# Optimization experiments

Hardware: AMD Instinct MI355X
Metric: run time of the kernel (lower is better)

The kernel has to match this reference:

```python
import jax, jax.numpy as jnp
import numpy as np

B, IN_DIM, HID, K, D = 16384, 1024, 2048, 8192, 128
COMMIT = 0.25


def setup_inputs() -> dict:
    key = jax.random.key(0)
    ks = jax.random.split(key, 10)
    s1 = 1.0 / np.sqrt(IN_DIM)
    s2 = 1.0 / np.sqrt(HID)
    s3 = 1.0 / np.sqrt(D)
    return {
        "x": jax.random.uniform(ks[0], (B, IN_DIM), dtype=jnp.float32),
        "W1": jax.random.normal(ks[1], (IN_DIM, HID), dtype=jnp.float32) * s1,
        "b1": jnp.zeros((HID,), jnp.float32),
        "W2": jax.random.normal(ks[2], (HID, D), dtype=jnp.float32) * s2,
        "b2": jnp.zeros((D,), jnp.float32),
        # torch init: uniform(-1/K, 1/K)
        "codebook": jax.random.uniform(ks[3], (K, D), dtype=jnp.float32, minval=-1.0 / K, maxval=1.0 / K),
        "W3": jax.random.normal(ks[4], (D, HID), dtype=jnp.float32) * s3,
        "b3": jnp.zeros((HID,), jnp.float32),
        "W4": jax.random.normal(ks[5], (HID, IN_DIM), dtype=jnp.float32) * s2,
        "b4": jnp.zeros((IN_DIM,), jnp.float32),
    }


def reference(x, W1, b1, W2, b2, codebook, W3, b3, W4, b4):
    # Encoder MLP: [B, IN] -> [B, D]
    h = jax.nn.relu(x @ W1 + b1)
    z = h @ W2 + b2                                   # [B, D]

    # Squared-distance to codebook: ||z||^2 - 2 z C^T + ||C||^2  -> [B, K]
    dists = (jnp.sum(z * z, axis=1, keepdims=True)
             - 2.0 * (z @ codebook.T)
             + jnp.sum(codebook * codebook, axis=1))
    indices = jnp.argmin(dists, axis=1)               # [B]
    z_q = codebook[indices]                            # [B, D]

    # Straight-through estimator
    z_q_st = z + jax.lax.stop_gradient(z_q - z)

    # Decoder MLP: [B, D] -> [B, IN]
    h2 = jax.nn.relu(z_q_st @ W3 + b3)
    recon = jax.nn.sigmoid(h2 @ W4 + b4)

    sg_zq = jax.lax.stop_gradient(z_q)
    mse = jnp.mean(jnp.square(sg_zq - z))
    loss = mse + COMMIT * mse
    return (recon, loss, indices)
```

## Files before the change

### kernel.cpp

```cpp
#include <hip/hip_runtime.h>
#include <hip/hip_bf16.h>


#define B_    16384
#define INDIM 1024
#define HID   2048
#define KCB   8192
#define DDIM  128

#define CAND_CAP 2000000u
#define LBUF_CAP 1024u

typedef __bf16    bf16x8   __attribute__((ext_vector_type(8)));
typedef float     floatx4  __attribute__((ext_vector_type(4)));
typedef double    doublex4 __attribute__((ext_vector_type(4)));
typedef _Float16  half8    __attribute__((ext_vector_type(8)));
typedef __fp16    fp16x2   __attribute__((ext_vector_type(2)));

#define XS 4096.0f
#define WS 8192.0f
#define SCALE_INV 2.9802322387695312e-08

__device__ __forceinline__ unsigned long long pack_key(float d, int code)
{
    unsigned int u = __float_as_uint(d);
    u = (u & 0x80000000u) ? ~u : (u | 0x80000000u);
    return ((unsigned long long)u << 32) | (unsigned int)code;
}

__device__ __forceinline__ unsigned packf(float d)
{
    unsigned u = __float_as_uint(d);
    return (u & 0x80000000u) ? ~u : (u | 0x80000000u);
}
__device__ __forceinline__ float unpackf(unsigned p)
{
    unsigned u = (p & 0x80000000u) ? (p ^ 0x80000000u) : ~p;
    return __uint_as_float(u);
}

__device__ __forceinline__ void gll16(const float* g, float* l)
{
    __builtin_amdgcn_global_load_lds(
        (const __attribute__((address_space(1))) void*)g,
        (__attribute__((address_space(3))) void*)l, 16, 0, 0);
}

template <int ACT, int PMASK>
__launch_bounds__(256)
__global__ void gemm_split_f16(const float* __restrict__ A, const _Float16* __restrict__ Bs_g,
                               const float* __restrict__ bias, float* __restrict__ Cout,
                               int M, int N, int K)
{
    __shared__ float    As[128 * 32];
    __shared__ _Float16 Bsh[64 * 64];

    const int t    = threadIdx.x;
    const int m0   = blockIdx.y * 128, n0 = blockIdx.x * 64;
    const int wave = t >> 6, lane = t & 63;
    const int wr   = (wave >> 1) * 64, wc = (wave & 1) * 32;
    const int quad = lane >> 4, l16 = lane & 15;
    const int lr   = lane >> 3;
    const int lcA  = ((lane & 7) ^ lr) * 4;
    const int slB  = lane & 7;
    const int lrB  = lane >> 3;

    floatx4  accf[4][2];
    doublex4 accd[4][2];
#pragma unroll
    for (int i = 0; i < 4; ++i)
#pragma unroll
        for (int j = 0; j < 2; ++j) {
            accf[i][j] = (floatx4){0.f, 0.f, 0.f, 0.f};
            accd[i][j] = (doublex4){0.0, 0.0, 0.0, 0.0};
        }

    const int NKT = K >> 5;
    for (int kt = 0; kt < NKT; ++kt) {
        const int k0 = kt << 5;
        __syncthreads();
#pragma unroll
        for (int s = 0; s < 4; ++s) {
            int r = wave * 32 + s * 8;
            gll16(A + (size_t)(m0 + r + lr) * K + k0 + lcA, &As[r * 32]);
        }
#pragma unroll
        for (int s = 0; s < 2; ++s) {
            int rb = wave * 16 + s * 8 + lrB;
            int ccs = slB ^ (lrB & 7);
            gll16((const float*)(Bs_g + (size_t)(n0 + rb) * (2 * K) + kt * 64 + ccs * 8),
                  (float*)&Bsh[(wave * 16 + s * 8) * 64]);
        }
        __syncthreads();

        half8 a1[4], a2[4];
#pragma unroll
        for (int i = 0; i < 4; ++i) {
            const int row = wr + i * 16 + l16;
            const int s0  = (2 * quad) ^ (row & 7);
            const int s1  = (2 * quad + 1) ^ (row & 7);
            floatx4 f0 = *(const floatx4*)&As[row * 32 + s0 * 4];
            floatx4 f1 = *(const floatx4*)&As[row * 32 + s1 * 4];
            union { half8 v; fp16x2 h[4]; } u1, u2;
            float sv[8];
#pragma unroll
            for (int q = 0; q < 4; ++q) sv[q] = f0[q] * XS;
#pragma unroll
            for (int q = 0; q < 4; ++q) sv[4 + q] = f1[q] * XS;
#pragma unroll
            for (int q = 0; q < 4; ++q) {
                fp16x2 hi = __builtin_amdgcn_cvt_pkrtz(sv[2 * q], sv[2 * q + 1]);
                u1.h[q] = hi;
                float r0 = sv[2 * q] - (float)hi[0];
                float r1 = sv[2 * q + 1] - (float)hi[1];
                u2.h[q] = __builtin_amdgcn_cvt_pkrtz(r0, r1);
            }
            a1[i] = u1.v; a2[i] = u2.v;
        }
        half8 b1[2], b2[2];
#pragma unroll
        for (int j = 0; j < 2; ++j) {
            const int row = wc + j * 16 + l16;
            b1[j] = *(const half8*)&Bsh[row * 64 + ((0 + quad) ^ (row & 7)) * 8];
            b2[j] = *(const half8*)&Bsh[row * 64 + ((4 + quad) ^ (row & 7)) * 8];
        }
#pragma unroll
        for (int i = 0; i < 4; ++i)
#pragma unroll
            for (int j = 0; j < 2; ++j)
                accf[i][j] = __builtin_amdgcn_mfma_f32_16x16x32_f16(a1[i], b1[j], accf[i][j], 0, 0, 0);
#pragma unroll
        for (int i = 0; i < 4; ++i)
#pragma unroll
            for (int j = 0; j < 2; ++j)
                accf[i][j] = __builtin_amdgcn_mfma_f32_16x16x32_f16(a1[i], b2[j], accf[i][j], 0, 0, 0);
#pragma unroll
        for (int i = 0; i < 4; ++i)
#pragma unroll
            for (int j = 0; j < 2; ++j)
                accf[i][j] = __builtin_amdgcn_mfma_f32_16x16x32_f16(a2[i], b1[j], accf[i][j], 0, 0, 0);

        if ((kt & PMASK) == PMASK) {
#pragma unroll
            for (int i = 0; i < 4; ++i)
#pragma unroll
                for (int j = 0; j < 2; ++j) {
#pragma unroll
                    for (int r = 0; r < 4; ++r)
                        accd[i][j][r] += (double)accf[i][j][r] * SCALE_INV;
                    accf[i][j] = (floatx4){0.f, 0.f, 0.f, 0.f};
                }
        }
    }
    if (NKT & PMASK) {
#pragma unroll
        for (int i = 0; i < 4; ++i)
#pragma unroll
            for (int j = 0; j < 2; ++j)
#pragma unroll
                for (int r = 0; r < 4; ++r)
                    accd[i][j][r] += (double)accf[i][j][r] * SCALE_INV;
    }

#pragma unroll
    for (int i = 0; i < 4; ++i)
#pragma unroll
        for (int j = 0; j < 2; ++j)
#pragma unroll
            for (int r = 0; r < 4; ++r) {
                int row = m0 + wr + i * 16 + quad * 4 + r;
                int col = n0 + wc + j * 16 + l16;
                float f = (float)(accd[i][j][r] + (double)bias[col]);
                if (ACT == 1) f = fmaxf(f, 0.f);
                Cout[(size_t)row * N + col] = f;
            }
}

template <int IM, int ACT, int PMASK, int SPLITOUT>
__launch_bounds__(256)
__global__ void gemm_split_pre(const _Float16* __restrict__ As_g, const _Float16* __restrict__ Bs_g,
                               const float* __restrict__ bias, void* __restrict__ Cp,
                               int M, int N, int K)
{
    __shared__ _Float16 Ash[IM * 32 * 64];
    __shared__ _Float16 Bsh[64 * 64];

    const int t    = threadIdx.x;
    const int nwg  = gridDim.x * gridDim.y;
    int lin = blockIdx.y * gridDim.x + blockIdx.x;
    lin = (lin & 7) * (nwg >> 3) + (lin >> 3);
    const int bx = lin % gridDim.x, by = lin / gridDim.x;
    const int m0   = by * (IM * 32), n0 = bx * 64;
    const int wave = t >> 6, lane = t & 63;
    const int wr   = (wave >> 1) * (IM * 16), wc = (wave & 1) * 32;
    const int quad = lane >> 4, l16 = lane & 15;
    const int slB  = lane & 7;
    const int lrB  = lane >> 3;
    const int ccs  = slB ^ (lrB & 7);

    floatx4  accf[IM][2];
    doublex4 accd[IM][2];
#pragma unroll
    for (int i = 0; i < IM; ++i)
#pragma unroll
        for (int j = 0; j < 2; ++j) {
            accf[i][j] = (floatx4){0.f, 0.f, 0.f, 0.f};
            accd[i][j] = (doublex4){0.0, 0.0, 0.0, 0.0};
        }

    const int NKT = K >> 5;
    for (int kt = 0; kt < NKT; ++kt) {
        __syncthreads();
#pragma unroll
        for (int s = 0; s < IM; ++s) {
            int ra = wave * (IM * 8) + s * 8 + lrB;
            gll16((const float*)(As_g + (size_t)(m0 + ra) * (2 * K) + kt * 64 + ccs * 8),
                  (float*)&Ash[(wave * (IM * 8) + s * 8) * 64]);
        }
#pragma unroll
        for (int s = 0; s < 2; ++s) {
            int rb = wave * 16 + s * 8 + lrB;
            gll16((const float*)(Bs_g + (size_t)(n0 + rb) * (2 * K) + kt * 64 + ccs * 8),
                  (float*)&Bsh[(wave * 16 + s * 8) * 64]);
        }
        __syncthreads();

        half8 a1[IM], a2[IM], b1[2], b2[2];
#pragma unroll
        for (int i = 0; i < IM; ++i) {
            const int row = wr + i * 16 + l16;
            a1[i] = *(const half8*)&Ash[row * 64 + ((0 + quad) ^ (row & 7)) * 8];
            a2[i] = *(const half8*)&Ash[row * 64 + ((4 + quad) ^ (row & 7)) * 8];
        }
#pragma unroll
        for (int j = 0; j < 2; ++j) {
            const int row = wc + j * 16 + l16;
            b1[j] = *(const half8*)&Bsh[row * 64 + ((0 + quad) ^ (row & 7)) * 8];
            b2[j] = *(const half8*)&Bsh[row * 64 + ((4 + quad) ^ (row & 7)) * 8];
        }
#pragma unroll
        for (int i = 0; i < IM; ++i)
#pragma unroll
            for (int j = 0; j < 2; ++j)
                accf[i][j] = __builtin_amdgcn_mfma_f32_16x16x32_f16(a1[i], b1[j], accf[i][j], 0, 0, 0);
#pragma unroll
        for (int i = 0; i < IM; ++i)
#pragma unroll
            for (int j = 0; j < 2; ++j)
                accf[i][j] = __builtin_amdgcn_mfma_f32_16x16x32_f16(a1[i], b2[j], accf[i][j], 0, 0, 0);
#pragma unroll
        for (int i = 0; i < IM; ++i)
#pragma unroll
            for (int j = 0; j < 2; ++j)
                accf[i][j] = __builtin_amdgcn_mfma_f32_16x16x32_f16(a2[i], b1[j], accf[i][j], 0, 0, 0);

        if ((kt & PMASK) == PMASK) {
#pragma unroll
            for (int i = 0; i < IM; ++i)
#pragma unroll
                for (int j = 0; j < 2; ++j) {
#pragma unroll
                    for (int r = 0; r < 4; ++r)
                        accd[i][j][r] += (double)accf[i][j][r] * SCALE_INV;
                    accf[i][j] = (floatx4){0.f, 0.f, 0.f, 0.f};
                }
        }
    }
    if (NKT & PMASK) {
#pragma unroll
        for (int i = 0; i < IM; ++i)
#pragma unroll
            for (int j = 0; j < 2; ++j)
#pragma unroll
                for (int r = 0; r < 4; ++r)
                    accd[i][j][r] += (double)accf[i][j][r] * SCALE_INV;
    }

#pragma unroll
    for (int i = 0; i < IM; ++i)
#pragma unroll
        for (int j = 0; j < 2; ++j)
#pragma unroll
            for (int r = 0; r < 4; ++r) {
                int row = m0 + wr + i * 16 + quad * 4 + r;
                int col = n0 + wc + j * 16 + l16;
                float f = (float)(accd[i][j][r] + (double)bias[col]);
                if (ACT == 1) f = fmaxf(f, 0.f);
                if (SPLITOUT == 1) {
                    float sv = f * XS;
                    _Float16 p0 = (_Float16)sv;
                    _Float16 p1 = (_Float16)(sv - (float)p0);
                    _Float16* hs = (_Float16*)Cp;
                    size_t base = (size_t)row * (2 * (size_t)N)
                                + (size_t)(col >> 5) * 64 + (col & 31);
                    hs[base]      = p0;
                    hs[base + 32] = p1;
                } else {
                    ((float*)Cp)[(size_t)row * N + col] = f;
                }
            }
}

template <int ACT>
__launch_bounds__(256)
__global__ void gemm_bf16_gll(const __bf16* __restrict__ A, const __bf16* __restrict__ BT,
                              const float* __restrict__ bias, void* __restrict__ Cp,
                              int M, int N, int K)
{
    __shared__ __bf16 Asm[128 * 32];
    __shared__ __bf16 Bsm[128 * 32];

    const int t    = threadIdx.x;
    const int nwg  = gridDim.x * gridDim.y;
    int lin = blockIdx.y * gridDim.x + blockIdx.x;
    lin = (lin & 7) * (nwg >> 3) + (lin >> 3);
    const int bx = lin % gridDim.x, by = lin / gridDim.x;
    const int m0   = by * 128, n0 = bx * 128;
    const int wave = t >> 6, lane = t & 63;
    const int wr   = (wave >> 1) * 64, wc = (wave & 1) * 64;
    const int quad = lane >> 4, l16 = lane & 15;
    const int srow = lane >> 2;
    const int schk = lane & 3;

    floatx4 acc[4][4];
#pragma unroll
    for (int i = 0; i < 4; ++i)
#pragma unroll
        for (int j = 0; j < 4; ++j) acc[i][j] = (floatx4){0.f, 0.f, 0.f, 0.f};

    for (int k0 = 0; k0 < K; k0 += 32) {
        __syncthreads();
#pragma unroll
        for (int s = 0; s < 2; ++s) {
            const int rbase = wave * 32 + s * 16;
            const int ra = rbase + srow;
            const int cs = (schk - (ra >> 1)) & 3;
            gll16((const float*)(A + (size_t)(m0 + ra) * K + k0 + cs * 8),
                  (float*)&Asm[rbase * 32]);
        }
#pragma unroll
        for (int s = 0; s < 2; ++s) {
            const int rbase = wave * 32 + s * 16;
            const int rb = rbase + srow;
            const int cs = (schk - (rb >> 1)) & 3;
            gll16((const float*)(BT + (size_t)(n0 + rb) * K + k0 + cs * 8),
                  (float*)&Bsm[rbase * 32]);
        }
        __syncthreads();

        bf16x8 af[4], bfr[4];
#pragma unroll
        for (int i = 0; i < 4; ++i) {
            const int rl = wr + i * 16 + l16;
            const int sl = (quad + (rl >> 1)) & 3;
            af[i] = *(const bf16x8*)&Asm[rl * 32 + sl * 8];
        }
#pragma unroll
        for (int j = 0; j < 4; ++j) {
            const int rl = wc + j * 16 + l16;
            const int sl = (quad + (rl >> 1)) & 3;
            bfr[j] = *(const bf16x8*)&Bsm[rl * 32 + sl * 8];
        }
#pragma unroll
        for (int i = 0; i < 4; ++i)
#pragma unroll
            for (int j = 0; j < 4; ++j)
                acc[i][j] = __builtin_amdgcn_mfma_f32_16x16x32_bf16(af[i], bfr[j], acc[i][j], 0, 0, 0);
    }

#pragma unroll
    for (int i = 0; i < 4; ++i)
#pragma unroll
        for (int j = 0; j < 4; ++j) {
            int col = n0 + wc + j * 16 + l16;
            float b = bias[col];
#pragma unroll
            for (int r = 0; r < 4; ++r) {
                int row = m0 + wr + i * 16 + quad * 4 + r;
                float v = acc[i][j][r] + b;
                if (ACT == 1) {
                    v = fmaxf(v, 0.f);
                    ((__bf16*)Cp)[(size_t)row * N + col] = (__bf16)v;
                } else {
                    v = 1.f / (1.f + __expf(-v));
                    ((float*)Cp)[(size_t)row * N + col] = v;
                }
            }
        }
}

__global__ void split_x(const float* __restrict__ in, _Float16* __restrict__ outS, int n8)
{
    int i = blockIdx.x * 256 + threadIdx.x;
    if (i >= n8) return;
    const int K = INDIM;
    int m  = i / (K / 8);
    int k8 = i % (K / 8);
    int k  = k8 * 8;
    const float* src = in + (size_t)m * K + k;
    floatx4 f0 = *(const floatx4*)(src);
    floatx4 f1 = *(const floatx4*)(src + 4);
    union { half8 v; fp16x2 h[4]; } u1, u2;
    float sv[8];
#pragma unroll
    for (int q = 0; q < 4; ++q) sv[q] = f0[q] * XS;
#pragma unroll
    for (int q = 0; q < 4; ++q) sv[4 + q] = f1[q] * XS;
#pragma unroll
    for (int q = 0; q < 4; ++q) {
        fp16x2 hi = __builtin_amdgcn_cvt_pkrtz(sv[2 * q], sv[2 * q + 1]);
        u1.h[q] = hi;
        float r0 = sv[2 * q] - (float)hi[0];
        float r1 = sv[2 * q + 1] - (float)hi[1];
        u2.h[q] = __builtin_amdgcn_cvt_pkrtz(r0, r1);
    }
    size_t base = (size_t)m * (2 * K) + (size_t)(k >> 5) * 64 + (k & 31);
    *(half8*)(outS + base)      = u1.v;
    *(half8*)(outS + base + 32) = u2.v;
}

__global__ void transpose_split_f16(const float* __restrict__ in, _Float16* __restrict__ outS,
                                    int K, int N)
{
    __shared__ float tile[32][33];
    int k0 = blockIdx.x * 32, n0 = blockIdx.y * 32;
    int tr = threadIdx.x >> 5, tc = threadIdx.x & 31;
#pragma unroll
    for (int s = 0; s < 4; ++s)
        tile[tr + 8 * s][tc] = in[(size_t)(k0 + tr + 8 * s) * N + n0 + tc];
    __syncthreads();
#pragma unroll
    for (int s = 0; s < 4; ++s) {
        int n = n0 + tr + 8 * s;
        int k = k0 + tc;
        float w = tile[tc][tr + 8 * s] * WS;
        _Float16 p0 = (_Float16)w;
        float r = w - (float)p0;
        _Float16 p1 = (_Float16)r;
        size_t base = (size_t)n * (2 * K) + (size_t)(k >> 5) * 64 + (k & 31);
        outS[base]      = p0;
        outS[base + 32] = p1;
    }
}

__global__ void rownorm_kernel(const float* __restrict__ M, float* __restrict__ nrm)
{
    int k = blockIdx.x * 4 + (threadIdx.x >> 6);
    int lane = threadIdx.x & 63;
    float2 c = *(const float2*)(M + (size_t)k * DDIM + lane * 2);
    float q0 = c.x * c.x;
    float q1 = c.y * c.y;
    double s = (double)q0 + (double)q1;
#pragma unroll
    for (int off = 32; off > 0; off >>= 1) s += __shfl_down(s, off);
    if (lane == 0) nrm[k] = (float)s;
}

__global__ void cnmax_kernel(const float* __restrict__ cn, float* __restrict__ out)
{
    __shared__ float red[4];
    int t = threadIdx.x;
    float m = 0.f;
    for (int i = t; i < KCB; i += 256) m = fmaxf(m, cn[i]);
#pragma unroll
    for (int off = 32; off > 0; off >>= 1) m = fmaxf(m, __shfl_down(m, off));
    if ((t & 63) == 0) red[t >> 6] = m;
    __syncthreads();
    if (t == 0) out[0] = fmaxf(fmaxf(red[0], red[1]), fmaxf(red[2], red[3]));
}

__global__ void cvt_half(const float* __restrict__ in, _Float16* __restrict__ out,
                         float scale, int n8)
{
    int i = blockIdx.x * 256 + threadIdx.x;
    if (i >= n8) return;
    const float4 a = *(const float4*)(in + (size_t)i * 8);
    const float4 b = *(const float4*)(in + (size_t)i * 8 + 4);
    half8 h;
    h[0] = (_Float16)(a.x * scale); h[1] = (_Float16)(a.y * scale);
    h[2] = (_Float16)(a.z * scale); h[3] = (_Float16)(a.w * scale);
    h[4] = (_Float16)(b.x * scale); h[5] = (_Float16)(b.y * scale);
    h[6] = (_Float16)(b.z * scale); h[7] = (_Float16)(b.w * scale);
    *(half8*)(out + (size_t)i * 8) = h;
}

__launch_bounds__(256)
__global__ void score_sweep3(const _Float16* __restrict__ zh, const _Float16* __restrict__ ch,
                             const float* __restrict__ nz32, const float* __restrict__ cn32,
                             const float* __restrict__ cnmaxp,
                             unsigned* __restrict__ listCnt, unsigned* __restrict__ list)
{
    __shared__ __align__(16) _Float16 Zs[32 * 128];
    __shared__ __align__(16) _Float16 Cs[128 * 128];
    __shared__ unsigned rowmin[32];
    __shared__ unsigned lbuf[LBUF_CAP];
    __shared__ unsigned lcnt, lbase;

    const int t    = threadIdx.x;
    int bid = blockIdx.x;
    bid = (bid & 7) * ((int)gridDim.x >> 3) + (bid >> 3);
    const int m0   = bid * 32;
    const int wave = t >> 6, lane = t & 63;
    const int quad = lane >> 4, l16 = lane & 15;
    const int srow = lane >> 4, sc = lane & 15;

    if (t == 0) lcnt = 0u;
    if (t < 32) rowmin[t] = 0xFFFFFFFFu;

#pragma unroll
    for (int s = 0; s < 2; ++s) {
        const int rbase = s * 16 + wave * 4;
        const int ra = rbase + srow;
        const int cs = sc ^ ((ra & 7) << 1);
        gll16((const float*)(zh + (size_t)(m0 + ra) * 128 + cs * 8),
              (float*)&Zs[rbase * 128]);
    }
    __syncthreads();

    half8 af[2][4];
#pragma unroll
    for (int i = 0; i < 2; ++i) {
        const int rl = i * 16 + l16;
#pragma unroll
        for (int ks = 0; ks < 4; ++ks) {
            const int cc = (ks * 4 + quad) ^ ((rl & 7) << 1);
            af[i][ks] = *(const half8*)&Zs[rl * 128 + cc * 8];
        }
    }

    const float cnm = *cnmaxp;
    float nzv[8], W[8];
    unsigned cachemin[8];
    int rowidx[8];
#pragma unroll
    for (int i = 0; i < 2; ++i)
#pragma unroll
        for (int r = 0; r < 4; ++r) {
            const int q = i * 4 + r;
            rowidx[q] = i * 16 + quad * 4 + r;
            const int grow = m0 + rowidx[q];
            nzv[q] = nz32[grow];
            W[q]   = 2.4e-3f * sqrtf(nzv[q] * cnm) + 6.0e-5f;
            cachemin[q] = 0xFFFFFFFFu;
        }

    for (int nt = 0; nt < KCB / 128; ++nt) {
        const int n0 = nt * 128;
        __syncthreads();
#pragma unroll
        for (int s = 0; s < 8; ++s) {
            const int rbase = s * 16 + wave * 4;
            const int ra = rbase + srow;
            const int cs = sc ^ ((ra & 7) << 1);
            gll16((const float*)(ch + (size_t)(n0 + ra) * 128 + cs * 8),
                  (float*)&Cs[rbase * 128]);
        }
        float cnj[2];
#pragma unroll
        for (int j = 0; j < 2; ++j)
            cnj[j] = cn32[n0 + wave * 32 + j * 16 + l16];
        __syncthreads();

        floatx4 acc[2][2];
#pragma unroll
        for (int i = 0; i < 2; ++i)
#pragma unroll
            for (int j = 0; j < 2; ++j) acc[i][j] = (floatx4){0.f, 0.f, 0.f, 0.f};
#pragma unroll
        for (int ks = 0; ks < 4; ++ks) {
            half8 bf[2];
#pragma unroll
            for (int j = 0; j < 2; ++j) {
                const int rl = wave * 32 + j * 16 + l16;
                const int cc = (ks * 4 + quad) ^ ((rl & 7) << 1);
                bf[j] = *(const half8*)&Cs[rl * 128 + cc * 8];
            }
#pragma unroll
            for (int i = 0; i < 2; ++i)
#pragma unroll
                for (int j = 0; j < 2; ++j)
                    acc[i][j] = __builtin_amdgcn_mfma_f32_16x16x32_f16(af[i][ks], bf[j], acc[i][j], 0, 0, 0);
        }

        float dv[8][2];
#pragma unroll
        for (int i = 0; i < 2; ++i)
#pragma unroll
            for (int r = 0; r < 4; ++r) {
                const int q = i * 4 + r;
#pragma unroll
                for (int j = 0; j < 2; ++j) {
                    float s = acc[i][j][r] * (1.0f / 4096.0f);
                    dv[q][j] = (nzv[q] - 2.0f * s) + cnj[j];
                }
                unsigned lp = packf(fminf(dv[q][0], dv[q][1]));
                if (lp < cachemin[q])
                    atomicMin(&rowmin[rowidx[q]], lp);
            }
        __syncthreads();

#pragma unroll
        for (int i = 0; i < 2; ++i)
#pragma unroll
            for (int r = 0; r < 4; ++r) {
                const int q = i * 4 + r;
                unsigned rp = rowmin[rowidx[q]];
                cachemin[q] = rp;
                const float thr = unpackf(rp) + W[q];
#pragma unroll
                for (int j = 0; j < 2; ++j) {
                    if (dv[q][j] <= thr) {
                        const int code = n0 + wave * 32 + j * 16 + l16;
                        unsigned ent = ((unsigned)(m0 + rowidx[q]) << 13) | (unsigned)code;
                        unsigned idx = atomicAdd(&lcnt, 1u);
                        if (idx < LBUF_CAP) lbuf[idx] = ent;
                        else {
                            unsigned g = atomicAdd(listCnt, 1u);
                            if (g < CAND_CAP) list[g] = ent;
                        }
                    }
                }
            }
    }

    __syncthreads();
    unsigned cnt = lcnt; if (cnt > LBUF_CAP) cnt = LBUF_CAP;
    if (t == 0) lbase = atomicAdd(listCnt, cnt);
    __syncthreads();
    for (unsigned e = t; e < cnt; e += 256) {
        unsigned g = lbase + e;
        if (g < CAND_CAP) list[g] = lbuf[e];
    }
}

__launch_bounds__(256)
__global__ void refine_kernel(const float* __restrict__ z, const float* __restrict__ cb,
                              const float* __restrict__ nz32, const float* __restrict__ cn32,
                              const unsigned* __restrict__ listCnt,
                              const unsigned* __restrict__ list,
                              unsigned long long* __restrict__ gbest)
{
    unsigned cnt = *listCnt;
    if (cnt > CAND_CAP) cnt = CAND_CAP;
    const int lane = threadIdx.x & 63;
    for (unsigned p = blockIdx.x * 4 + (threadIdx.x >> 6); p < cnt; p += gridDim.x * 4) {
        const unsigned e = list[p];
        const int r = (int)(e >> 13), k = (int)(e & 8191u);
        float2 zv = *(const float2*)(z  + (size_t)r * DDIM + lane * 2);
        float2 cv = *(const float2*)(cb + (size_t)k * DDIM + lane * 2);
        double s = (double)zv.x * (double)cv.x + (double)zv.y * (double)cv.y;
#pragma unroll
        for (int off = 32; off > 0; off >>= 1) s += __shfl_down(s, off);
        if (lane == 0) {
            float s32 = (float)s;
            float d = (nz32[r] - 2.0f * s32) + cn32[k];
            atomicMin(&gbest[r], pack_key(d, k));
        }
    }
}

__global__ void init_gbest(unsigned long long* __restrict__ g,
                           double* __restrict__ acc, unsigned* __restrict__ cnt)
{
    g[blockIdx.x * 256 + threadIdx.x] = ~0ull;
    if (blockIdx.x == 0 && threadIdx.x == 0) { *acc = 0.0; *cnt = 0u; }
}

__global__ void gather_zq_loss(const float* __restrict__ z, const float* __restrict__ cb,
                               const unsigned long long* __restrict__ gbest,
                               __bf16* __restrict__ zqb, double* __restrict__ acc)
{
    int r = blockIdx.x * 4 + (threadIdx.x >> 6);
    int lane = threadIdx.x & 63;
    int k = (int)(gbest[r] & 0xffffffffull);
    float2 zv = *(const float2*)(z  + (size_t)r * DDIM + lane * 2);
    float2 cv = *(const float2*)(cb + (size_t)k * DDIM + lane * 2);
    __bf16 b0 = (__bf16)cv.x, b1 = (__bf16)cv.y;
    zqb[(size_t)r * DDIM + lane * 2]     = b0;
    zqb[(size_t)r * DDIM + lane * 2 + 1] = b1;
    double dx = (double)cv.x - (double)zv.x, dy = (double)cv.y - (double)zv.y;
    double s = dx * dx + dy * dy;
#pragma unroll
    for (int off = 32; off > 0; off >>= 1) s += __shfl_down(s, off);
    if (lane == 0) atomicAdd(acc, s);
}

__global__ void finalize_kernel(const unsigned long long* __restrict__ gbest,
                                const double* __restrict__ acc, float* __restrict__ out)
{
    int tid = blockIdx.x * 256 + threadIdx.x;
    if (tid < B_) out[16777217 + tid] = (float)(int)(gbest[tid] & 0xffffffffull);
    if (tid == 0) out[16777216] = (float)((*acc) * 1.25 / (double)(B_ * DDIM));
}

__global__ void transpose_to_bf16(const float* __restrict__ in, __bf16* __restrict__ outT,
                                  int K, int N)
{
    __shared__ float tile[32][33];
    int k0 = blockIdx.x * 32, n0 = blockIdx.y * 32;
    int tr = threadIdx.x >> 5, tc = threadIdx.x & 31;
#pragma unroll
    for (int s = 0; s < 4; ++s)
        tile[tr + 8 * s][tc] = in[(size_t)(k0 + tr + 8 * s) * N + n0 + tc];
    __syncthreads();
#pragma unroll
    for (int s = 0; s < 4; ++s)
        outT[(size_t)(n0 + tr + 8 * s) * K + k0 + tc] = (__bf16)tile[tc][tr + 8 * s];
}

extern "C" void kernel_launch(void* const* d_in, const int* in_sizes, int n_in,
                              void* d_out, int out_size, void* d_ws, size_t ws_size,
                              hipStream_t stream)
{
    const float* x  = (const float*)d_in[0];
    const float* W1 = (const float*)d_in[1];
    const float* b1 = (const float*)d_in[2];
    const float* W2 = (const float*)d_in[3];
    const float* b2 = (const float*)d_in[4];
    const float* cb = (const float*)d_in[5];
    const float* W3 = (const float*)d_in[6];
    const float* b3 = (const float*)d_in[7];
    const float* W4 = (const float*)d_in[8];
    const float* b4 = (const float*)d_in[9];
    float* out = (float*)d_out;

    char* ws = (char*)d_ws;
    _Float16* hs = (_Float16*)(ws);
    float*  h    = (float*)(ws);
    __bf16* h2b  = (__bf16*)(ws + 16777216ull);
    _Float16* zh  = (_Float16*)(ws);
    _Float16* chh = (_Float16*)(ws + 4194304ull);
    unsigned* list = (unsigned*)(ws + 8388608ull);
    float*  z32  = (float*)(ws + 134217728ull);
    __bf16* zqb  = (__bf16*)(ws + 142606336ull);
    _Float16* W1s = (_Float16*)(ws + 142606336ull);
    float*  nz32 = (float*)(ws + 150994944ull);
    float*  cn32 = (float*)(ws + 151060480ull);
    unsigned long long* gbest = (unsigned long long*)(ws + 151093248ull);
    double* acc  = (double*)(ws + 151224320ull);
    float*  cnmax   = (float*)(ws + 151224328ull);
    unsigned* listCnt = (unsigned*)(ws + 151224332ull);
    __bf16* W3t  = (__bf16*)(ws + 151228416ull);
    __bf16* W4t  = (__bf16*)(ws + 151752704ull);
    _Float16* W2s = (_Float16*)(ws + 155947008ull);

    const unsigned long long XS_OFF = 157286400ull;
    _Float16* xs = (_Float16*)(ws + XS_OFF);
    const bool pre_split_x = (ws_size >= XS_OFF + 67108864ull);

    init_gbest<<<B_ / 256, 256, 0, stream>>>(gbest, acc, listCnt);
    rownorm_kernel<<<KCB / 4, 256, 0, stream>>>(cb, cn32);
    cnmax_kernel<<<1, 256, 0, stream>>>(cn32, cnmax);
    transpose_to_bf16<<<dim3(DDIM / 32, HID / 32), 256, 0, stream>>>(W3, W3t, DDIM, HID);
    transpose_to_bf16<<<dim3(HID / 32, INDIM / 32), 256, 0, stream>>>(W4, W4t, HID, INDIM);
    transpose_split_f16<<<dim3(INDIM / 32, HID / 32), 256, 0, stream>>>(W1, W1s, INDIM, HID);
    transpose_split_f16<<<dim3(HID / 32, DDIM / 32), 256, 0, stream>>>(W2, W2s, HID, DDIM);

    if (pre_split_x) {
        split_x<<<(B_ * INDIM / 8) / 256, 256, 0, stream>>>(x, xs, B_ * INDIM / 8);
        gemm_split_pre<4, 1, 3, 1><<<dim3(HID / 64, B_ / 128), 256, 0, stream>>>(
            xs, W1s, b1, (void*)hs, B_, HID, INDIM);
        gemm_split_pre<2, 0, 1, 0><<<dim3(DDIM / 64, B_ / 64), 256, 0, stream>>>(
            hs, W2s, b2, (void*)z32, B_, DDIM, HID);
    } else {
        gemm_split_f16<1, 3><<<dim3(HID / 64, B_ / 128), 256, 0, stream>>>(
            x, W1s, b1, h, B_, HID, INDIM);
        gemm_split_f16<0, 1><<<dim3(DDIM / 64, B_ / 128), 256, 0, stream>>>(
            h, W2s, b2, z32, B_, DDIM, HID);
    }
    rownorm_kernel<<<B_ / 4, 256, 0, stream>>>(z32, nz32);

    cvt_half<<<(B_ * DDIM / 8) / 256, 256, 0, stream>>>(z32, zh, 1.0f, B_ * DDIM / 8);
    cvt_half<<<(KCB * DDIM / 8) / 256, 256, 0, stream>>>(cb, chh, 4096.0f, KCB * DDIM / 8);
    score_sweep3<<<B_ / 32, 256, 0, stream>>>(
        zh, chh, nz32, cn32, cnmax, listCnt, list);
    refine_kernel<<<1024, 256, 0, stream>>>(z32, cb, nz32, cn32, listCnt, list, gbest);

    gather_zq_loss<<<B_ / 4, 256, 0, stream>>>(z32, cb, gbest, zqb, acc);
    gemm_bf16_gll<1><<<dim3(HID / 128, B_ / 128), 256, 0, stream>>>(
        zqb, W3t, b3, (void*)h2b, B_, HID, DDIM);
    gemm_bf16_gll<2><<<dim3(INDIM / 128, B_ / 128), 256, 0, stream>>>(
        h2b, W4t, b4, (void*)out, B_, INDIM, HID);

    finalize_kernel<<<B_ / 256, 256, 0, stream>>>(gbest, acc, out);
}
```

Before: 947.1 us.

## Widen score sweep codebook tile, fuse z norm with half conversion, toggle swizzle

The score sweep kernel now stages 256 codebook rows per iteration instead of 128, and each wave computes a 16x64 tile. This halves the number of sync/threshold passes and gives more MFMA work per barrier, at the cost of doubled LDS for Cs, which may lower occupancy. The z row-norm and fp16 conversion are merged into one kernel so z is read once. The block-index swizzle is also made a template flag and switched off for the first encoder GEMM.

```diff
diff --git a/kernel.cpp b/kernel.cpp
--- a/kernel.cpp
+++ b/kernel.cpp
@@ -176,7 +176,7 @@
             }
 }
 
-template <int IM, int ACT, int PMASK, int SPLITOUT>
+template <int IM, int ACT, int PMASK, int SPLITOUT, int SWZ>
 __launch_bounds__(256)
 __global__ void gemm_split_pre(const _Float16* __restrict__ As_g, const _Float16* __restrict__ Bs_g,
                                const float* __restrict__ bias, void* __restrict__ Cp,
@@ -186,10 +186,15 @@
     __shared__ _Float16 Bsh[64 * 64];
 
     const int t    = threadIdx.x;
-    const int nwg  = gridDim.x * gridDim.y;
-    int lin = blockIdx.y * gridDim.x + blockIdx.x;
-    lin = (lin & 7) * (nwg >> 3) + (lin >> 3);
-    const int bx = lin % gridDim.x, by = lin / gridDim.x;
+    int bx, by;
+    if (SWZ) {
+        const int nwg = gridDim.x * gridDim.y;
+        int lin = blockIdx.y * gridDim.x + blockIdx.x;
+        lin = (lin & 7) * (nwg >> 3) + (lin >> 3);
+        bx = lin % gridDim.x; by = lin / gridDim.x;
+    } else {
+        bx = blockIdx.x; by = blockIdx.y;
+    }
     const int m0   = by * (IM * 32), n0 = bx * 64;
     const int wave = t >> 6, lane = t & 63;
     const int wr   = (wave >> 1) * (IM * 16), wc = (wave & 1) * 32;
@@ -456,6 +461,22 @@
     if (lane == 0) nrm[k] = (float)s;
 }
 
+__global__ void rownorm_cvt_z(const float* __restrict__ M, float* __restrict__ nrm,
+                              _Float16* __restrict__ outh)
+{
+    int k = blockIdx.x * 4 + (threadIdx.x >> 6);
+    int lane = threadIdx.x & 63;
+    float2 c = *(const float2*)(M + (size_t)k * DDIM + lane * 2);
+    outh[(size_t)k * DDIM + lane * 2]     = (_Float16)c.x;
+    outh[(size_t)k * DDIM + lane * 2 + 1] = (_Float16)c.y;
+    float q0 = c.x * c.x;
+    float q1 = c.y * c.y;
+    double s = (double)q0 + (double)q1;
+#pragma unroll
+    for (int off = 32; off > 0; off >>= 1) s += __shfl_down(s, off);
+    if (lane == 0) nrm[k] = (float)s;
+}
+
 __global__ void cnmax_kernel(const float* __restrict__ cn, float* __restrict__ out)
 {
     __shared__ float red[4];
@@ -491,7 +512,7 @@
                              unsigned* __restrict__ listCnt, unsigned* __restrict__ list)
 {
     __shared__ __align__(16) _Float16 Zs[32 * 128];
-    __shared__ __align__(16) _Float16 Cs[128 * 128];
+    __shared__ __align__(16) _Float16 Cs[256 * 128];
     __shared__ unsigned rowmin[32];
     __shared__ unsigned lbuf[LBUF_CAP];
     __shared__ unsigned lcnt, lbase;
@@ -544,56 +565,58 @@
             cachemin[q] = 0xFFFFFFFFu;
         }
 
-    for (int nt = 0; nt < KCB / 128; ++nt) {
-        const int n0 = nt * 128;
+    for (int nt = 0; nt < KCB / 256; ++nt) {
+        const int n0 = nt * 256;
         __syncthreads();
 #pragma unroll
-        for (int s = 0; s < 8; ++s) {
+        for (int s = 0; s < 16; ++s) {
             const int rbase = s * 16 + wave * 4;
             const int ra = rbase + srow;
             const int cs = sc ^ ((ra & 7) << 1);
             gll16((const float*)(ch + (size_t)(n0 + ra) * 128 + cs * 8),
                   (float*)&Cs[rbase * 128]);
         }
-        float cnj[2];
-#pragma unroll
-        for (int j = 0; j < 2; ++j)
-            cnj[j] = cn32[n0 + wave * 32 + j * 16 + l16];
+        float cnj[4];
+#pragma unroll
+        for (int j = 0; j < 4; ++j)
+            cnj[j] = cn32[n0 + wave * 64 + j * 16 + l16];
         __syncthreads();
 
-        floatx4 acc[2][2];
+        floatx4 acc[2][4];
 #pragma unroll
         for (int i = 0; i < 2; ++i)
 #pragma unroll
-            for (int j = 0; j < 2; ++j) acc[i][j] = (floatx4){0.f, 0.f, 0.f, 0.f};
+            for (int j = 0; j < 4; ++j) acc[i][j] = (floatx4){0.f, 0.f, 0.f, 0.f};
 #pragma unroll
         for (int ks = 0; ks < 4; ++ks) {
-            half8 bf[2];
-#pragma unroll
-            for (int j = 0; j < 2; ++j) {
-                const int rl = wave * 32 + j * 16 + l16;
+            half8 bf[4];
+#pragma unroll
+            for (int j = 0; j < 4; ++j) {
+                const int rl = wave * 64 + j * 16 + l16;
                 const int cc = (ks * 4 + quad) ^ ((rl & 7) << 1);
                 bf[j] = *(const half8*)&Cs[rl * 128 + cc * 8];
             }
 #pragma unroll
             for (int i = 0; i < 2; ++i)
 #pragma unroll
-                for (int j = 0; j < 2; ++j)
+                for (int j = 0; j < 4; ++j)
                     acc[i][j] = __builtin_amdgcn_mfma_f32_16x16x32_f16(af[i][ks], bf[j], acc[i][j], 0, 0, 0);
         }
 
-        float dv[8][2];
+        float dv[8][4];
 #pragma unroll
         for (int i = 0; i < 2; ++i)
 #pragma unroll
             for (int r = 0; r < 4; ++r) {
                 const int q = i * 4 + r;
-#pragma unroll
-                for (int j = 0; j < 2; ++j) {
+                float lmin = 3.4e38f;
+#pragma unroll
+                for (int j = 0; j < 4; ++j) {
                     float s = acc[i][j][r] * (1.0f / 4096.0f);
                     dv[q][j] = (nzv[q] - 2.0f * s) + cnj[j];
+                    lmin = fminf(lmin, dv[q][j]);
                 }
-                unsigned lp = packf(fminf(dv[q][0], dv[q][1]));
+                unsigned lp = packf(lmin);
                 if (lp < cachemin[q])
                     atomicMin(&rowmin[rowidx[q]], lp);
             }
@@ -608,9 +631,9 @@
                 cachemin[q] = rp;
                 const float thr = unpackf(rp) + W[q];
 #pragma unroll
-                for (int j = 0; j < 2; ++j) {
+                for (int j = 0; j < 4; ++j) {
                     if (dv[q][j] <= thr) {
-                        const int code = n0 + wave * 32 + j * 16 + l16;
+                        const int code = n0 + wave * 64 + j * 16 + l16;
                         unsigned ent = ((unsigned)(m0 + rowidx[q]) << 13) | (unsigned)code;
                         unsigned idx = atomicAdd(&lcnt, 1u);
                         if (idx < LBUF_CAP) lbuf[idx] = ent;
@@ -758,9 +781,9 @@
 
     if (pre_split_x) {
         split_x<<<(B_ * INDIM / 8) / 256, 256, 0, stream>>>(x, xs, B_ * INDIM / 8);
-        gemm_split_pre<4, 1, 3, 1><<<dim3(HID / 64, B_ / 128), 256, 0, stream>>>(
+        gemm_split_pre<4, 1, 3, 1, 0><<<dim3(HID / 64, B_ / 128), 256, 0, stream>>>(
             xs, W1s, b1, (void*)hs, B_, HID, INDIM);
-        gemm_split_pre<2, 0, 1, 0><<<dim3(DDIM / 64, B_ / 64), 256, 0, stream>>>(
+        gemm_split_pre<2, 0, 1, 0, 1><<<dim3(DDIM / 64, B_ / 64), 256, 0, stream>>>(
             hs, W2s, b2, (void*)z32, B_, DDIM, HID);
     } else {
         gemm_split_f16<1, 3><<<dim3(HID / 64, B_ / 128), 256, 0, stream>>>(
@@ -768,10 +791,9 @@
         gemm_split_f16<0, 1><<<dim3(DDIM / 64, B_ / 128), 256, 0, stream>>>(
             h, W2s, b2, z32, B_, DDIM, HID);
     }
-    rownorm_kernel<<<B_ / 4, 256, 0, stream>>>(z32, nz32);
-
-    cvt_half<<<(B_ * DDIM / 8) / 256, 256, 0, stream>>>(z32, zh, 1.0f, B_ * DDIM / 8);
+    rownorm_cvt_z<<<B_ / 4, 256, 0, stream>>>(z32, nz32, zh);
     cvt_half<<<(KCB * DDIM / 8) / 256, 256, 0, stream>>>(cb, chh, 4096.0f, KCB * DDIM / 8);
+
     score_sweep3<<<B_ / 32, 256, 0, stream>>>(
         zh, chh, nz32, cn32, cnmax, listCnt, list);
     refine_kernel<<<1024, 256, 0, stream>>>(z32, cb, nz32, cn32, listCnt, list, gbest);
```

New measurement: 928.6 us. No clear change (-2.0%).
